# Kernel optimization log

Measured on AMD Instinct MI355X. Metric: run time of the kernel, lower is better.

The kernel has to match this reference:

```python
import jax, jax.numpy as jnp
import numpy as np

B, T, D, H, O = 1024, 512, 64, 64, 32


def setup_inputs() -> dict:
    key = jax.random.key(0)
    ks = jax.random.split(key, 12)
    s = 1.0 / np.sqrt(H)  # torch LSTM/Linear default init scale
    u = lambda k, shape: jax.random.uniform(k, shape, jnp.float32, -s, s)
    return {
        "x": jax.random.normal(ks[0], (B, T, D), jnp.float32),
        # layer 0 (PyTorch gate order: i, f, g, o stacked along first dim)
        "w_ih0": u(ks[1], (4 * H, D)),
        "w_hh0": u(ks[2], (4 * H, H)),
        "b_ih0": u(ks[3], (4 * H,)),
        "b_hh0": u(ks[4], (4 * H,)),
        # layer 1
        "w_ih1": u(ks[5], (4 * H, H)),
        "w_hh1": u(ks[6], (4 * H, H)),
        "b_ih1": u(ks[7], (4 * H,)),
        "b_hh1": u(ks[8], (4 * H,)),
        # final linear head
        "fc_w": u(ks[9], (O, H)),
        "fc_b": u(ks[10], (O,)),
    }


def lstm_layer(x, w_ih, w_hh, b_ih, b_hh):
    """Single batch-first LSTM layer, PyTorch gate order (i, f, g, o)."""
    Bb = x.shape[0]
    Hh = w_hh.shape[1]
    # precompute input contribution for all timesteps: (B, T, 4H)
    pre = jnp.einsum('btd,gd->btg', x, w_ih) + b_ih + b_hh

    def step(carry, p_t):  # p_t: (B, 4H)
        h, c = carry
        gates = p_t + h @ w_hh.T
        i, f, g, o = jnp.split(gates, 4, axis=-1)
        c = jax.nn.sigmoid(f) * c + jax.nn.sigmoid(i) * jnp.tanh(g)
        h = jax.nn.sigmoid(o) * jnp.tanh(c)
        return (h, c), h

    h0 = jnp.zeros((Bb, Hh), x.dtype)
    (_, _), hs = jax.lax.scan(step, (h0, h0), jnp.swapaxes(pre, 0, 1))
    return jnp.swapaxes(hs, 0, 1)  # (B, T, H)


def reference(x, w_ih0, w_hh0, b_ih0, b_hh0, w_ih1, w_hh1, b_ih1, b_hh1, fc_w, fc_b):
    h1 = lstm_layer(x, w_ih0, w_hh0, b_ih0, b_hh0)
    h2 = lstm_layer(h1, w_ih1, w_hh1, b_ih1, b_hh1)
    last = h2[:, -1, :]  # (B, H)
    return jax.nn.softplus(last @ fc_w.T + fc_b)  # (B, O)
```

## Files before the change

### kernel.cpp

```cpp
#include <hip/hip_runtime.h>
#include <hip/hip_bf16.h>
#include <math.h>

#define BB 1024
#define TT 512
#define OO 32
#define MM 4
#define NBLK (BB/MM)

typedef __attribute__((ext_vector_type(8))) short short8;
typedef __attribute__((ext_vector_type(4))) float f32x4;

#define MFMA __builtin_amdgcn_mfma_f32_16x16x32_bf16
#define LOG2E 1.4426950408889634f
#define K2    2.8853900817779268f

#define BAR() asm volatile("s_waitcnt lgkmcnt(0)\n\ts_barrier" ::: "memory")

__device__ __forceinline__ float exp2f_(float x) {
#if __has_builtin(__builtin_amdgcn_exp2f)
    return __builtin_amdgcn_exp2f(x);
#else
    float r; asm("v_exp_f32 %0, %1" : "=v"(r) : "v"(x)); return r;
#endif
}

__device__ __forceinline__ ushort f2bf(float f) {
    union { float f; unsigned u; } v; v.f = f;
    unsigned r = v.u + 0x7FFF + ((v.u >> 16) & 1);
    return (ushort)(r >> 16);
}
__device__ __forceinline__ float bf2f(ushort u) {
    union { unsigned u; float f; } v; v.u = ((unsigned)u) << 16; return v.f;
}
__device__ __forceinline__ unsigned pkbf(float a, float b) {
    union { float f; unsigned u; } x, y; x.f = a; y.f = b;
    return __builtin_amdgcn_perm(y.u + 0x8000u, x.u + 0x8000u, 0x07060302u);
}
__device__ __forceinline__ short8 pack8(const float4& a, const float4& b) {
    union { unsigned u[4]; short8 s; } r;
    r.u[0] = pkbf(a.x, a.y); r.u[1] = pkbf(a.z, a.w);
    r.u[2] = pkbf(b.x, b.y); r.u[3] = pkbf(b.z, b.w);
    return r.s;
}

__global__ __launch_bounds__(512)
void lstm_f256(const float* __restrict__ x,
               const float* __restrict__ w_ih0,
               const float* __restrict__ w_hh0,
               const float* __restrict__ b_ih0,
               const float* __restrict__ b_hh0,
               const float* __restrict__ w_ih1,
               const float* __restrict__ w_hh1,
               const float* __restrict__ b_ih1,
               const float* __restrict__ b_hh1,
               const float* __restrict__ fc_w,
               const float* __restrict__ fc_b,
               float* __restrict__ out)
{
    __shared__ ushort h0s[2][16][72];
    __shared__ ushort h1s[2][16][72];
    __shared__ float  gsh[8][4][16][4];

    const int tid  = threadIdx.x;
    const int wv   = tid >> 6;
    const bool gB  = (wv >= 4);
    const int u    = wv & 3;
    const int ln   = tid & 63;
    const int l15  = ln & 15;
    const int quad = ln >> 4;
    const int b0   = blockIdx.x * MM;
    const int hq   = 16 * u + l15;

    const float* wih = gB ? w_ih1 : w_ih0;
    const float* whh = gB ? w_hh1 : w_hh0;
    const float* bih = gB ? b_ih1 : b_ih0;
    const float* bhh = gB ? b_hh1 : b_hh0;

    short8 bfrag[4][4];
    f32x4  bias4[4];
#pragma unroll
    for (int g = 0; g < 4; ++g) {
        const float sc = (g == 2) ? K2 : -LOG2E;
        const int col = 64 * g + 16 * u + l15;
        const float bv = (bih[col] + bhh[col]) * sc;
        bias4[g] = (f32x4){bv, bv, bv, bv};
#pragma unroll
        for (int kt = 0; kt < 4; ++kt) {
            const int kb = kt * 32 + quad * 8;
            const float* src = (kb < 64) ? (wih + col * 64 + kb)
                                         : (whh + col * 64 + (kb - 64));
            const float4 v0 = *(const float4*)src;
            const float4 v1 = *(const float4*)(src + 4);
            short8 b;
            b[0] = (short)f2bf(v0.x * sc); b[1] = (short)f2bf(v0.y * sc);
            b[2] = (short)f2bf(v0.z * sc); b[3] = (short)f2bf(v0.w * sc);
            b[4] = (short)f2bf(v1.x * sc); b[5] = (short)f2bf(v1.y * sc);
            b[6] = (short)f2bf(v1.z * sc); b[7] = (short)f2bf(v1.w * sc);
            bfrag[g][kt] = b;
        }
    }

    const int xr = (l15 < MM) ? l15 : (MM - 1);
    const size_t xoff = ((size_t)(b0 + xr) * TT) * 64 + quad * 8;
    float4 xfA0, xfA1, xfA2, xfA3, xfB0, xfB1, xfB2, xfB3;
    f32x4 pre[4];

#define ISSUE(t_, S)                                                          \
    if ((t_) < TT) {                                                          \
        const float* p = x + xoff + (size_t)(t_) * 64;                        \
        xf##S##0 = *(const float4*)p;        xf##S##1 = *(const float4*)(p + 4);  \
        xf##S##2 = *(const float4*)(p + 32); xf##S##3 = *(const float4*)(p + 36); \
    }

    for (int i = tid; i < 2 * 16 * 72; i += 512) {
        ((ushort*)h0s)[i] = 0;
        ((ushort*)h1s)[i] = 0;
    }

    float cc = 0.f;
    if (!gB) {
        ISSUE(0, A);
        ISSUE(1, B);
        const short8 xlo = pack8(xfA0, xfA1);
        const short8 xhi = pack8(xfA2, xfA3);
#pragma unroll
        for (int g = 0; g < 4; ++g)
            pre[g] = MFMA(xhi, bfrag[g][1],
                          MFMA(xlo, bfrag[g][0], bias4[g], 0, 0, 0), 0, 0, 0);
    }
    BAR();

#define CELL1(HD, NXT)                                                        \
    {                                                                         \
        const float yi = gsh[wv][0][l15][quad];                               \
        const float yf = gsh[wv][1][l15][quad];                               \
        const float yg = gsh[wv][2][l15][quad];                               \
        const float yo = gsh[wv][3][l15][quad];                               \
        const float Ef = exp2f_(yf);                                          \
        const float Ei = exp2f_(yi);                                          \
        const float Eg = exp2f_(fminf(yg, 80.f));                             \
        const float sf = __builtin_amdgcn_rcpf(1.f + Ef);                     \
        const float rd = __builtin_amdgcn_rcpf((1.f + Ei) * (1.f + Eg));      \
        cc = sf * cc + (Eg - 1.f) * rd;                                       \
        const float Ec = exp2f_(fminf(cc * K2, 80.f));                        \
        const float Eo = exp2f_(yo);                                          \
        const float r2 = __builtin_amdgcn_rcpf((1.f + Eo) * (1.f + Ec));      \
        union { float f; unsigned uu; } hv; hv.f = (Ec - 1.f) * r2;           \
        HD[NXT][quad][hq] = (ushort)((hv.uu + 0x8000u) >> 16);                \
    }

#define STEP(t_, CUR, NXT, USE, LD, DOA, DOB)                                 \
    {                                                                         \
        if (!gB) {                                                            \
            if (DOA) {                                                        \
                const short8 a2 = *(const short8*)&h0s[CUR][l15][quad * 8];   \
                const short8 a3 = *(const short8*)&h0s[CUR][l15][32 + quad * 8]; \
                f32x4 acc[4];                                                 \
                _Pragma("unroll")                                             \
                for (int g = 0; g < 4; ++g)                                   \
                    acc[g] = MFMA(a3, bfrag[g][3],                            \
                                  MFMA(a2, bfrag[g][2], pre[g], 0,0,0), 0,0,0); \
                if (quad == 0) {                                              \
                    _Pragma("unroll")                                         \
                    for (int g = 0; g < 4; ++g)                               \
                        *(f32x4*)&gsh[wv][g][l15][0] = acc[g];                \
                }                                                             \
                ISSUE((t_) + 2, LD);                                          \
                CELL1(h0s, NXT);                                              \
                if ((t_) + 1 < TT) {                                          \
                    const short8 xlo = pack8(xf##USE##0, xf##USE##1);         \
                    const short8 xhi = pack8(xf##USE##2, xf##USE##3);         \
                    _Pragma("unroll")                                         \
                    for (int g = 0; g < 4; ++g)                               \
                        pre[g] = MFMA(xhi, bfrag[g][1],                       \
                                      MFMA(xlo, bfrag[g][0], bias4[g], 0,0,0), 0,0,0); \
                }                                                             \
            }                                                                 \
        } else {                                                              \
            if (DOB) {                                                        \
                const short8 a0 = *(const short8*)&h0s[CUR][l15][quad * 8];   \
                const short8 a1 = *(const short8*)&h0s[CUR][l15][32 + quad * 8]; \
                const short8 a2 = *(const short8*)&h1s[CUR][l15][quad * 8];   \
                const short8 a3 = *(const short8*)&h1s[CUR][l15][32 + quad * 8]; \
                f32x4 acc[4];                                                 \
                _Pragma("unroll")                                             \
                for (int g = 0; g < 4; ++g) {                                 \
                    f32x4 a = bias4[g];                                       \
                    a = MFMA(a0, bfrag[g][0], a, 0, 0, 0);                    \
                    a = MFMA(a1, bfrag[g][1], a, 0, 0, 0);                    \
                    a = MFMA(a2, bfrag[g][2], a, 0, 0, 0);                    \
                    a = MFMA(a3, bfrag[g][3], a, 0, 0, 0);                    \
                    acc[g] = a;                                               \
                }                                                             \
                if (quad == 0) {                                              \
                    _Pragma("unroll")                                         \
                    for (int g = 0; g < 4; ++g)                               \
                        *(f32x4*)&gsh[wv][g][l15][0] = acc[g];                \
                }                                                             \
                CELL1(h1s, NXT);                                              \
            }                                                                 \
        }                                                                     \
        BAR();                                                                \
    }

    STEP(0, 0, 1, B, A, 1, 0)
    for (int tb = 1; tb + 2 < TT; tb += 2) {
        STEP(tb,     1, 0, A, B, 1, 1)
        STEP(tb + 1, 0, 1, B, A, 1, 1)
    }
    STEP(TT - 1, 1, 0, A, B, 1, 1)
    STEP(TT, 0, 1, B, A, 0, 1)
#undef STEP
#undef CELL1
#undef ISSUE

    if (tid < MM * OO) {
        const int row = tid >> 5, o = tid & 31;
        float a = fc_b[o];
#pragma unroll
        for (int j = 0; j < 64; ++j)
            a = fmaf(fc_w[o * 64 + j], bf2f(h1s[1][row][j]), a);
        out[(size_t)(b0 + row) * OO + o] =
            fmaxf(a, 0.0f) + log1pf(__expf(-fabsf(a)));
    }
}

extern "C" void kernel_launch(void* const* d_in, const int* in_sizes, int n_in,
                              void* d_out, int out_size, void* d_ws, size_t ws_size,
                              hipStream_t stream) {
    const float* x     = (const float*)d_in[0];
    const float* w_ih0 = (const float*)d_in[1];
    const float* w_hh0 = (const float*)d_in[2];
    const float* b_ih0 = (const float*)d_in[3];
    const float* b_hh0 = (const float*)d_in[4];
    const float* w_ih1 = (const float*)d_in[5];
    const float* w_hh1 = (const float*)d_in[6];
    const float* b_ih1 = (const float*)d_in[7];
    const float* b_hh1 = (const float*)d_in[8];
    const float* fc_w  = (const float*)d_in[9];
    const float* fc_b  = (const float*)d_in[10];
    float* out = (float*)d_out;

    lstm_f256<<<dim3(NBLK), dim3(512), 0, stream>>>(
        x, w_ih0, w_hh0, b_ih0, b_hh0,
        w_ih1, w_hh1, b_ih1, b_hh1, fc_w, fc_b, out);
}
```

Before: 555.3 us.

## Replicate batch rows across MFMA A-rows to read gates directly from registers

Each batch row (4 per block) is now replicated across 4 lanes of the MFMA A operand via xr = l15>>2, so every lane's output element [0] already holds its own gate pre-activation. This removes the gsh shared-memory round trip and its LDS write/read per step. The dependent MFMA chains are also split into two independent accumulators summed afterwards, which shortens the serial MFMA latency on the recurrent critical path. The cost is that MFMA rows are fully redundant and one extra add per gate is needed, and the h buffers shrink to 4 rows.

```diff
diff --git a/kernel.cpp b/kernel.cpp
--- a/kernel.cpp
+++ b/kernel.cpp
@@ -1,5 +1,4 @@
 #include <hip/hip_runtime.h>
-#include <hip/hip_bf16.h>
 #include <math.h>
 
 #define BB 1024
@@ -58,9 +57,8 @@
                const float* __restrict__ fc_b,
                float* __restrict__ out)
 {
-    __shared__ ushort h0s[2][16][72];
-    __shared__ ushort h1s[2][16][72];
-    __shared__ float  gsh[8][4][16][4];
+    __shared__ __align__(16) ushort h0s[2][4][80];
+    __shared__ __align__(16) ushort h1s[2][4][80];
 
     const int tid  = threadIdx.x;
     const int wv   = tid >> 6;
@@ -71,6 +69,7 @@
     const int quad = ln >> 4;
     const int b0   = blockIdx.x * MM;
     const int hq   = 16 * u + l15;
+    const int xr   = l15 >> 2;
 
     const float* wih = gB ? w_ih1 : w_ih0;
     const float* whh = gB ? w_hh1 : w_hh0;
@@ -101,10 +100,10 @@
         }
     }
 
-    const int xr = (l15 < MM) ? l15 : (MM - 1);
     const size_t xoff = ((size_t)(b0 + xr) * TT) * 64 + quad * 8;
     float4 xfA0, xfA1, xfA2, xfA3, xfB0, xfB1, xfB2, xfB3;
     f32x4 pre[4];
+    const f32x4 z4 = (f32x4){0.f, 0.f, 0.f, 0.f};
 
 #define ISSUE(t_, S)                                                          \
     if ((t_) < TT) {                                                          \
@@ -113,7 +112,7 @@
         xf##S##2 = *(const float4*)(p + 32); xf##S##3 = *(const float4*)(p + 36); \
     }
 
-    for (int i = tid; i < 2 * 16 * 72; i += 512) {
+    for (int i = tid; i < 2 * 4 * 80; i += 512) {
         ((ushort*)h0s)[i] = 0;
         ((ushort*)h1s)[i] = 0;
     }
@@ -131,20 +130,16 @@
     }
     BAR();
 
-#define CELL1(HD, NXT)                                                        \
+#define CELL1(YI, YF, YG, YO, HD, NXT)                                        \
     {                                                                         \
-        const float yi = gsh[wv][0][l15][quad];                               \
-        const float yf = gsh[wv][1][l15][quad];                               \
-        const float yg = gsh[wv][2][l15][quad];                               \
-        const float yo = gsh[wv][3][l15][quad];                               \
-        const float Ef = exp2f_(yf);                                          \
-        const float Ei = exp2f_(yi);                                          \
-        const float Eg = exp2f_(fminf(yg, 80.f));                             \
+        const float Ef = exp2f_(YF);                                          \
+        const float Ei = exp2f_(YI);                                          \
+        const float Eg = exp2f_(fminf((YG), 80.f));                           \
         const float sf = __builtin_amdgcn_rcpf(1.f + Ef);                     \
         const float rd = __builtin_amdgcn_rcpf((1.f + Ei) * (1.f + Eg));      \
         cc = sf * cc + (Eg - 1.f) * rd;                                       \
         const float Ec = exp2f_(fminf(cc * K2, 80.f));                        \
-        const float Eo = exp2f_(yo);                                          \
+        const float Eo = exp2f_(YO);                                          \
         const float r2 = __builtin_amdgcn_rcpf((1.f + Eo) * (1.f + Ec));      \
         union { float f; unsigned uu; } hv; hv.f = (Ec - 1.f) * r2;           \
         HD[NXT][quad][hq] = (ushort)((hv.uu + 0x8000u) >> 16);                \
@@ -154,20 +149,20 @@
     {                                                                         \
         if (!gB) {                                                            \
             if (DOA) {                                                        \
-                const short8 a2 = *(const short8*)&h0s[CUR][l15][quad * 8];   \
-                const short8 a3 = *(const short8*)&h0s[CUR][l15][32 + quad * 8]; \
-                f32x4 acc[4];                                                 \
+                const short8 a2 = *(const short8*)&h0s[CUR][xr][quad * 8];    \
+                const short8 a3 = *(const short8*)&h0s[CUR][xr][32 + quad * 8]; \
+                f32x4 aA[4], aB[4];                                           \
                 _Pragma("unroll")                                             \
-                for (int g = 0; g < 4; ++g)                                   \
-                    acc[g] = MFMA(a3, bfrag[g][3],                            \
-                                  MFMA(a2, bfrag[g][2], pre[g], 0,0,0), 0,0,0); \
-                if (quad == 0) {                                              \
-                    _Pragma("unroll")                                         \
-                    for (int g = 0; g < 4; ++g)                               \
-                        *(f32x4*)&gsh[wv][g][l15][0] = acc[g];                \
+                for (int g = 0; g < 4; ++g) {                                 \
+                    aA[g] = MFMA(a2, bfrag[g][2], pre[g], 0, 0, 0);           \
+                    aB[g] = MFMA(a3, bfrag[g][3], z4, 0, 0, 0);               \
                 }                                                             \
                 ISSUE((t_) + 2, LD);                                          \
-                CELL1(h0s, NXT);                                              \
+                const float yi = aA[0][0] + aB[0][0];                         \
+                const float yf = aA[1][0] + aB[1][0];                         \
+                const float yg = aA[2][0] + aB[2][0];                         \
+                const float yo = aA[3][0] + aB[3][0];                         \
+                CELL1(yi, yf, yg, yo, h0s, NXT);                              \
                 if ((t_) + 1 < TT) {                                          \
                     const short8 xlo = pack8(xf##USE##0, xf##USE##1);         \
                     const short8 xhi = pack8(xf##USE##2, xf##USE##3);         \
@@ -179,26 +174,23 @@
             }                                                                 \
         } else {                                                              \
             if (DOB) {                                                        \
-                const short8 a0 = *(const short8*)&h0s[CUR][l15][quad * 8];   \
-                const short8 a1 = *(const short8*)&h0s[CUR][l15][32 + quad * 8]; \
-                const short8 a2 = *(const short8*)&h1s[CUR][l15][quad * 8];   \
-                const short8 a3 = *(const short8*)&h1s[CUR][l15][32 + quad * 8]; \
-                f32x4 acc[4];                                                 \
+                const short8 a0 = *(const short8*)&h0s[CUR][xr][quad * 8];    \
+                const short8 a1 = *(const short8*)&h0s[CUR][xr][32 + quad * 8]; \
+                const short8 a2 = *(const short8*)&h1s[CUR][xr][quad * 8];    \
+                const short8 a3 = *(const short8*)&h1s[CUR][xr][32 + quad * 8]; \
+                f32x4 aA[4], aB[4];                                           \
                 _Pragma("unroll")                                             \
                 for (int g = 0; g < 4; ++g) {                                 \
-                    f32x4 a = bias4[g];                                       \
-                    a = MFMA(a0, bfrag[g][0], a, 0, 0, 0);                    \
-                    a = MFMA(a1, bfrag[g][1], a, 0, 0, 0);                    \
-                    a = MFMA(a2, bfrag[g][2], a, 0, 0, 0);                    \
-                    a = MFMA(a3, bfrag[g][3], a, 0, 0, 0);                    \
-                    acc[g] = a;                                               \
+                    aA[g] = MFMA(a1, bfrag[g][1],                             \
+                                 MFMA(a0, bfrag[g][0], bias4[g], 0, 0, 0), 0, 0, 0); \
+                    aB[g] = MFMA(a3, bfrag[g][3],                             \
+                                 MFMA(a2, bfrag[g][2], z4, 0, 0, 0), 0, 0, 0); \
                 }                                                             \
-                if (quad == 0) {                                              \
-                    _Pragma("unroll")                                         \
-                    for (int g = 0; g < 4; ++g)                               \
-                        *(f32x4*)&gsh[wv][g][l15][0] = acc[g];                \
-                }                                                             \
-                CELL1(h1s, NXT);                                              \
+                const float yi = aA[0][0] + aB[0][0];                         \
+                const float yf = aA[1][0] + aB[1][0];                         \
+                const float yg = aA[2][0] + aB[2][0];                         \
+                const float yo = aA[3][0] + aB[3][0];                         \
+                CELL1(yi, yf, yg, yo, h1s, NXT);                              \
             }                                                                 \
         }                                                                     \
         BAR();                                                                \
```

New measurement: 485.3 us. -12.6%, faster.
